# Kernel tuning notes

Hardware: AMD Instinct MI355X
Metric: run time of the kernel (lower is better)

## Reference

```python
import jax, jax.numpy as jnp
import numpy as np

N_NODES = 50000
N_EDGES = 800000
D_IN = 128
D_OUT = 128


def setup_inputs() -> dict:
    key = jax.random.key(0)
    k1, k2, k3, k4, k5 = jax.random.split(key, 5)
    H = jax.random.normal(k1, (N_NODES, D_IN), dtype=jnp.float32)
    stdv = 1.0 / np.sqrt(D_OUT)
    W = jax.random.uniform(k2, (D_IN, D_OUT), dtype=jnp.float32, minval=-stdv, maxval=stdv)
    bias = jnp.zeros((D_OUT,), dtype=jnp.float32)
    edge_vals = jax.random.uniform(k3, (N_EDGES,), dtype=jnp.float32)
    edge_rows = jax.random.randint(k4, (N_EDGES,), 0, N_NODES, dtype=jnp.int32)
    edge_cols = jax.random.randint(k5, (N_EDGES,), 0, N_NODES, dtype=jnp.int32)
    return {"H": H, "W": W, "bias": bias, "edge_vals": edge_vals,
            "edge_rows": edge_rows, "edge_cols": edge_cols}


def reference(H, W, bias, edge_vals, edge_rows, edge_cols):
    # H' = relu(A @ (H W) + b), A given as COO edge list (rows, cols, vals)
    n = H.shape[0]
    HW = H @ W  # [N, D_out]
    # SpMM: out[r] = sum_{e: row(e)=r} val(e) * HW[col(e)]
    msgs = edge_vals[:, None] * HW[edge_cols]  # [E, D_out]
    out = jax.ops.segment_sum(msgs, edge_rows, num_segments=n)
    out = out + bias
    return jax.nn.relu(out)
```

## Files before the change

kernel.cpp:

```cpp
#include <hip/hip_runtime.h>

#define D 128
#define BM 64
#define NBB 256
#define BINSH 6
#define MAXBINS 1024
#define CAPB 1536

typedef __attribute__((ext_vector_type(8))) short bf16x8;
typedef __attribute__((ext_vector_type(4))) float f32x4;

__device__ __forceinline__ unsigned short f2bf(float f) {
    unsigned u = __float_as_uint(f);
    u = (u + 0x7FFFu + ((u >> 16) & 1u)) >> 16;
    return (unsigned short)u;
}
__device__ __forceinline__ float bf2f(unsigned short h) {
    return __uint_as_float(((unsigned)h) << 16);
}

__global__ __launch_bounds__(128) void k_prepw(const float* __restrict__ W,
                                               unsigned short* __restrict__ Wt,
                                               int* __restrict__ gcnt, int nbins) {
    int nn = blockIdx.x, k = threadIdx.x;
    Wt[nn * D + k] = f2bf(W[k * D + nn]);
    int gtid = blockIdx.x * 128 + threadIdx.x;
    for (int i = gtid; i < nbins * 16; i += 128 * D) gcnt[i] = 0;
}

__global__ __launch_bounds__(256) void k_gemm_bin(const float* __restrict__ H,
                                                  const unsigned short* __restrict__ Wt,
                                                  unsigned short* __restrict__ HWb,
                                                  int n,
                                                  const int* __restrict__ rows,
                                                  const int* __restrict__ cols,
                                                  const float* __restrict__ vals,
                                                  int* __restrict__ gcnt,
                                                  int2* __restrict__ segs,
                                                  int E, int nbins, int nbb) {
    __shared__ unsigned short sA[BM * D];
    __shared__ unsigned short sB[D * D];
    const int tid = threadIdx.x;
    const int row0 = blockIdx.x * BM;

#pragma unroll
    for (int s = 0; s < 8; ++s) {
        int idx = s * 256 + tid;
        int nn = idx >> 4, cc = idx & 15;
        bf16x8 v = *reinterpret_cast<const bf16x8*>(&Wt[(size_t)idx * 8]);
        *reinterpret_cast<bf16x8*>(&sB[nn * D + ((cc ^ (nn & 7)) * 8)]) = v;
    }
#pragma unroll
    for (int s = 0; s < 4; ++s) {
        int idx = s * 256 + tid;
        int r = idx >> 4, cc = idx & 15;
        int row = row0 + r;
        float4 u0 = make_float4(0.f, 0.f, 0.f, 0.f), u1 = u0;
        if (row < n) {
            const float4* p = reinterpret_cast<const float4*>(&H[(size_t)row * D + cc * 8]);
            u0 = p[0]; u1 = p[1];
        }
        bf16x8 v;
        v[0] = (short)f2bf(u0.x); v[1] = (short)f2bf(u0.y);
        v[2] = (short)f2bf(u0.z); v[3] = (short)f2bf(u0.w);
        v[4] = (short)f2bf(u1.x); v[5] = (short)f2bf(u1.y);
        v[6] = (short)f2bf(u1.z); v[7] = (short)f2bf(u1.w);
        *reinterpret_cast<bf16x8*>(&sA[r * D + ((cc ^ (r & 7)) * 8)]) = v;
    }
    __syncthreads();

    const int w = tid >> 6, l = tid & 63;
    const int lr = l & 15, lq = l >> 4;
    f32x4 acc[8];
#pragma unroll
    for (int ct = 0; ct < 8; ++ct) acc[ct] = (f32x4){0.f, 0.f, 0.f, 0.f};

#pragma unroll
    for (int ks = 0; ks < 4; ++ks) {
        const int arow = w * 16 + lr;
        const int acc_c = (ks * 4 + lq) ^ (arow & 7);
        bf16x8 a = *reinterpret_cast<const bf16x8*>(&sA[arow * D + acc_c * 8]);
#pragma unroll
        for (int ct = 0; ct < 8; ++ct) {
            const int brow = ct * 16 + lr;
            const int bcc = (ks * 4 + lq) ^ (brow & 7);
            bf16x8 b = *reinterpret_cast<const bf16x8*>(&sB[brow * D + bcc * 8]);
            acc[ct] = __builtin_amdgcn_mfma_f32_16x16x32_bf16(a, b, acc[ct], 0, 0, 0);
        }
    }

#pragma unroll
    for (int ct = 0; ct < 8; ++ct) {
#pragma unroll
        for (int i = 0; i < 4; ++i) {
            int row = row0 + w * 16 + lq * 4 + i;
            int col = ct * 16 + lr;
            if (row < n) HWb[(size_t)row * D + col] = f2bf(acc[ct][i]);
        }
    }

    if (blockIdx.x < (unsigned)nbb) {
        __syncthreads();
        int* lcnt = reinterpret_cast<int*>(sA);
        int* loff = lcnt + MAXBINS;
        int chunk = (E + nbb - 1) / nbb;
        int s = blockIdx.x * chunk;
        int epos = s + chunk; if (epos > E) epos = E;
        for (int i = tid; i < nbins; i += 256) lcnt[i] = 0;
        __syncthreads();
        for (int e = s + tid; e < epos; e += 256)
            atomicAdd(&lcnt[rows[e] >> BINSH], 1);
        __syncthreads();
        for (int i = tid; i < nbins; i += 256) {
            int c = lcnt[i];
            int base = c ? atomicAdd(&gcnt[i * 16], c) : 0;
            loff[i] = i * CAPB + base;
            lcnt[i] = 0;
        }
        __syncthreads();
        for (int e = s + tid; e < epos; e += 256) {
            int r = rows[e];
            int c = cols[e];
            float v = vals[e];
            int bin = r >> BINSH;
            int p = atomicAdd(&lcnt[bin], 1);
            int pos = loff[bin] + p;
            if (pos < (bin + 1) * CAPB)
                segs[pos] = make_int2(((r & 63) << 16) | c, __float_as_int(v));
        }
    }
}

__global__ __launch_bounds__(512) void k_spmm(const unsigned short* __restrict__ HWb,
                                              const int* __restrict__ gcnt,
                                              const int2* __restrict__ segs,
                                              const float* __restrict__ bias,
                                              float* __restrict__ out, int n) {
    __shared__ int2 sent[CAPB];
    __shared__ int lcnt[64];
    __shared__ int loff[64];
    __shared__ int lcur[64];
    const int b = blockIdx.x;
    int cnt = gcnt[b * 16];
    if (cnt > CAPB) cnt = CAPB;
    const int2* seg = segs + (size_t)b * CAPB;

    if (threadIdx.x < 64) lcnt[threadIdx.x] = 0;
    __syncthreads();
    int2 er[3];
#pragma unroll
    for (int k = 0; k < 3; ++k) {
        int i = threadIdx.x + k * 512;
        if (i < cnt) {
            er[k] = seg[i];
            atomicAdd(&lcnt[((unsigned)er[k].x) >> 16], 1);
        }
    }
    __syncthreads();
    if (threadIdx.x < 64) {
        int v = lcnt[threadIdx.x];
        int inc = v;
#pragma unroll
        for (int o = 1; o < 64; o <<= 1) {
            int t = __shfl_up(inc, o);
            if (threadIdx.x >= o) inc += t;
        }
        loff[threadIdx.x] = inc - v;
        lcur[threadIdx.x] = inc - v;
    }
    __syncthreads();
#pragma unroll
    for (int k = 0; k < 3; ++k) {
        int i = threadIdx.x + k * 512;
        if (i < cnt) {
            int p = atomicAdd(&lcur[((unsigned)er[k].x) >> 16], 1);
            sent[p] = er[k];
        }
    }
    __syncthreads();

    const int w = threadIdx.x >> 6, lane = threadIdx.x & 63;
    const unsigned c2 = 2 * lane;
    const float2 bb = *reinterpret_cast<const float2*>(&bias[c2]);

    for (int rr = w; rr < 64; rr += 8) {
        int row = b * 64 + rr;
        if (row >= n) break;
        int s = loff[rr];
        int deg = lcnt[rr];
        float a0 = 0.f, a1 = 0.f, b0 = 0.f, b1 = 0.f;
        int t = 0;
        for (; t + 8 <= deg; t += 8) {
            int2 e0 = sent[s + t],     e1 = sent[s + t + 1];
            int2 e2 = sent[s + t + 2], e3 = sent[s + t + 3];
            int2 e4 = sent[s + t + 4], e5 = sent[s + t + 5];
            int2 e6 = sent[s + t + 6], e7 = sent[s + t + 7];
            unsigned m0 = *reinterpret_cast<const unsigned*>(&HWb[(size_t)(e0.x & 0xFFFF) * D + c2]);
            unsigned m1 = *reinterpret_cast<const unsigned*>(&HWb[(size_t)(e1.x & 0xFFFF) * D + c2]);
            unsigned m2 = *reinterpret_cast<const unsigned*>(&HWb[(size_t)(e2.x & 0xFFFF) * D + c2]);
            unsigned m3 = *reinterpret_cast<const unsigned*>(&HWb[(size_t)(e3.x & 0xFFFF) * D + c2]);
            unsigned m4 = *reinterpret_cast<const unsigned*>(&HWb[(size_t)(e4.x & 0xFFFF) * D + c2]);
            unsigned m5 = *reinterpret_cast<const unsigned*>(&HWb[(size_t)(e5.x & 0xFFFF) * D + c2]);
            unsigned m6 = *reinterpret_cast<const unsigned*>(&HWb[(size_t)(e6.x & 0xFFFF) * D + c2]);
            unsigned m7 = *reinterpret_cast<const unsigned*>(&HWb[(size_t)(e7.x & 0xFFFF) * D + c2]);
            float v0 = __int_as_float(e0.y), v1 = __int_as_float(e1.y);
            float v2 = __int_as_float(e2.y), v3 = __int_as_float(e3.y);
            float v4 = __int_as_float(e4.y), v5 = __int_as_float(e5.y);
            float v6 = __int_as_float(e6.y), v7 = __int_as_float(e7.y);
            a0 += v0 * bf2f((unsigned short)(m0 & 0xFFFF));
            a1 += v0 * bf2f((unsigned short)(m0 >> 16));
            b0 += v1 * bf2f((unsigned short)(m1 & 0xFFFF));
            b1 += v1 * bf2f((unsigned short)(m1 >> 16));
            a0 += v2 * bf2f((unsigned short)(m2 & 0xFFFF));
            a1 += v2 * bf2f((unsigned short)(m2 >> 16));
            b0 += v3 * bf2f((unsigned short)(m3 & 0xFFFF));
            b1 += v3 * bf2f((unsigned short)(m3 >> 16));
            a0 += v4 * bf2f((unsigned short)(m4 & 0xFFFF));
            a1 += v4 * bf2f((unsigned short)(m4 >> 16));
            b0 += v5 * bf2f((unsigned short)(m5 & 0xFFFF));
            b1 += v5 * bf2f((unsigned short)(m5 >> 16));
            a0 += v6 * bf2f((unsigned short)(m6 & 0xFFFF));
            a1 += v6 * bf2f((unsigned short)(m6 >> 16));
            b0 += v7 * bf2f((unsigned short)(m7 & 0xFFFF));
            b1 += v7 * bf2f((unsigned short)(m7 >> 16));
        }
        for (; t < deg; ++t) {
            int2 e = sent[s + t];
            unsigned m = *reinterpret_cast<const unsigned*>(&HWb[(size_t)(e.x & 0xFFFF) * D + c2]);
            float v = __int_as_float(e.y);
            a0 += v * bf2f((unsigned short)(m & 0xFFFF));
            a1 += v * bf2f((unsigned short)(m >> 16));
        }
        float2 o;
        o.x = fmaxf(a0 + b0 + bb.x, 0.f);
        o.y = fmaxf(a1 + b1 + bb.y, 0.f);
        *reinterpret_cast<float2*>(&out[(size_t)row * D + c2]) = o;
    }
}

__global__ void k_init_bias(const float* __restrict__ bias, float* __restrict__ out, int n) {
    int i = blockIdx.x * blockDim.x + threadIdx.x;
    if (i < n * D) out[i] = bias[i & (D - 1)];
}
__global__ void k_scatter(const unsigned short* __restrict__ HWb, const int* __restrict__ rows,
                          const int* __restrict__ cols, const float* __restrict__ vals,
                          float* __restrict__ out, int E) {
    int e = blockIdx.x * 2 + (threadIdx.x >> 7);
    int j = threadIdx.x & (D - 1);
    if (e < E) {
        int r = rows[e];
        int c = cols[e];
        float v = vals[e];
        atomicAdd(&out[(size_t)r * D + j], v * bf2f(HWb[(size_t)c * D + j]));
    }
}
__global__ void k_relu(float* __restrict__ out, int n) {
    int i = blockIdx.x * blockDim.x + threadIdx.x;
    if (i < n * D) out[i] = fmaxf(out[i], 0.f);
}

extern "C" void kernel_launch(void* const* d_in, const int* in_sizes, int n_in,
                              void* d_out, int out_size, void* d_ws, size_t ws_size,
                              hipStream_t stream) {
    const float* H         = (const float*)d_in[0];
    const float* W         = (const float*)d_in[1];
    const float* bias      = (const float*)d_in[2];
    const float* edge_vals = (const float*)d_in[3];
    const int*   edge_rows = (const int*)d_in[4];
    const int*   edge_cols = (const int*)d_in[5];
    float* out = (float*)d_out;

    const int n = in_sizes[0] / D;
    const int E = in_sizes[3];
    const int gblocks = (n + BM - 1) / BM;
    const int nbins = (n + 63) >> BINSH;
    const int nbb = (gblocks < NBB) ? gblocks : NBB;

    char* ws = (char*)d_ws;
    unsigned short* HWb = (unsigned short*)ws; ws += (size_t)n * D * sizeof(unsigned short);
    unsigned short* Wt  = (unsigned short*)ws; ws += (size_t)D * D * sizeof(unsigned short);
    int* gcnt = (int*)ws;            ws += (size_t)nbins * 16 * sizeof(int);
    int2* segs = (int2*)ws;          ws += (size_t)nbins * CAPB * sizeof(int2);
    size_t need_full = (size_t)(ws - (char*)d_ws);

    k_prepw<<<D, D, 0, stream>>>(W, Wt, gcnt, nbins);

    if (ws_size >= need_full && n < 65536 && nbins <= MAXBINS) {
        k_gemm_bin<<<gblocks, 256, 0, stream>>>(H, Wt, HWb, n,
                                                edge_rows, edge_cols, edge_vals,
                                                gcnt, segs, E, nbins, nbb);
        k_spmm<<<nbins, 512, 0, stream>>>(HWb, gcnt, segs, bias, out, n);
    } else {
        k_gemm_bin<<<gblocks, 256, 0, stream>>>(H, Wt, HWb, n,
                                                edge_rows, edge_cols, edge_vals,
                                                (int*)d_ws, (int2*)d_ws, 0, nbins, 0);
        k_init_bias<<<((size_t)n * D + 255) / 256, 256, 0, stream>>>(bias, out, n);
        k_scatter<<<(E + 1) / 2, 256, 0, stream>>>(HWb, edge_rows, edge_cols, edge_vals, out, E);
        k_relu<<<((size_t)n * D + 255) / 256, 256, 0, stream>>>(out, n);
    }
}
```

Baseline: 73.59 us.

## Split GEMM K loop into two halves to shrink LDS and vectorize output stores

The fused GEMM+binning kernel now loads H and W in two K-halves of 64, halving the shared-memory footprint (sA/sB) so more blocks can be resident per CU. It also swaps the MFMA operand order so each lane holds four consecutive output columns of one row, letting the HW output be written as 8-byte ushort4 stores instead of scalar 2-byte stores. The cost is an extra barrier and a second load phase per block. The LDS region reused by the binning step is also smaller, which may constrain the lcnt/loff arrays.

```diff
diff --git a/kernel.cpp b/kernel.cpp
--- a/kernel.cpp
+++ b/kernel.cpp
@@ -38,64 +38,72 @@
                                                   int* __restrict__ gcnt,
                                                   int2* __restrict__ segs,
                                                   int E, int nbins, int nbb) {
-    __shared__ unsigned short sA[BM * D];
-    __shared__ unsigned short sB[D * D];
+    __shared__ unsigned short sA[BM * 64];
+    __shared__ unsigned short sB[D * 64];
     const int tid = threadIdx.x;
     const int row0 = blockIdx.x * BM;
-
-#pragma unroll
-    for (int s = 0; s < 8; ++s) {
-        int idx = s * 256 + tid;
-        int nn = idx >> 4, cc = idx & 15;
-        bf16x8 v = *reinterpret_cast<const bf16x8*>(&Wt[(size_t)idx * 8]);
-        *reinterpret_cast<bf16x8*>(&sB[nn * D + ((cc ^ (nn & 7)) * 8)]) = v;
-    }
-#pragma unroll
-    for (int s = 0; s < 4; ++s) {
-        int idx = s * 256 + tid;
-        int r = idx >> 4, cc = idx & 15;
-        int row = row0 + r;
-        float4 u0 = make_float4(0.f, 0.f, 0.f, 0.f), u1 = u0;
-        if (row < n) {
-            const float4* p = reinterpret_cast<const float4*>(&H[(size_t)row * D + cc * 8]);
-            u0 = p[0]; u1 = p[1];
-        }
-        bf16x8 v;
-        v[0] = (short)f2bf(u0.x); v[1] = (short)f2bf(u0.y);
-        v[2] = (short)f2bf(u0.z); v[3] = (short)f2bf(u0.w);
-        v[4] = (short)f2bf(u1.x); v[5] = (short)f2bf(u1.y);
-        v[6] = (short)f2bf(u1.z); v[7] = (short)f2bf(u1.w);
-        *reinterpret_cast<bf16x8*>(&sA[r * D + ((cc ^ (r & 7)) * 8)]) = v;
-    }
-    __syncthreads();
-
     const int w = tid >> 6, l = tid & 63;
     const int lr = l & 15, lq = l >> 4;
+
     f32x4 acc[8];
 #pragma unroll
     for (int ct = 0; ct < 8; ++ct) acc[ct] = (f32x4){0.f, 0.f, 0.f, 0.f};
 
 #pragma unroll
-    for (int ks = 0; ks < 4; ++ks) {
-        const int arow = w * 16 + lr;
-        const int acc_c = (ks * 4 + lq) ^ (arow & 7);
-        bf16x8 a = *reinterpret_cast<const bf16x8*>(&sA[arow * D + acc_c * 8]);
-#pragma unroll
-        for (int ct = 0; ct < 8; ++ct) {
-            const int brow = ct * 16 + lr;
-            const int bcc = (ks * 4 + lq) ^ (brow & 7);
-            bf16x8 b = *reinterpret_cast<const bf16x8*>(&sB[brow * D + bcc * 8]);
-            acc[ct] = __builtin_amdgcn_mfma_f32_16x16x32_bf16(a, b, acc[ct], 0, 0, 0);
-        }
-    }
-
-#pragma unroll
-    for (int ct = 0; ct < 8; ++ct) {
-#pragma unroll
-        for (int i = 0; i < 4; ++i) {
-            int row = row0 + w * 16 + lq * 4 + i;
-            int col = ct * 16 + lr;
-            if (row < n) HWb[(size_t)row * D + col] = f2bf(acc[ct][i]);
+    for (int kt = 0; kt < 2; ++kt) {
+        if (kt) __syncthreads();
+#pragma unroll
+        for (int s = 0; s < 4; ++s) {
+            int idx = s * 256 + tid;
+            int r = idx >> 3, cc = idx & 7;
+            bf16x8 v = *reinterpret_cast<const bf16x8*>(&Wt[(size_t)r * D + kt * 64 + cc * 8]);
+            *reinterpret_cast<bf16x8*>(&sB[r * 64 + ((cc ^ (r & 7)) * 8)]) = v;
+        }
+#pragma unroll
+        for (int s = 0; s < 2; ++s) {
+            int idx = s * 256 + tid;
+            int r = idx >> 3, cc = idx & 7;
+            int row = row0 + r;
+            float4 u0 = make_float4(0.f, 0.f, 0.f, 0.f), u1 = u0;
+            if (row < n) {
+                const float4* p = reinterpret_cast<const float4*>(
+                    &H[(size_t)row * D + kt * 64 + cc * 8]);
+                u0 = p[0]; u1 = p[1];
+            }
+            bf16x8 v;
+            v[0] = (short)f2bf(u0.x); v[1] = (short)f2bf(u0.y);
+            v[2] = (short)f2bf(u0.z); v[3] = (short)f2bf(u0.w);
+            v[4] = (short)f2bf(u1.x); v[5] = (short)f2bf(u1.y);
+            v[6] = (short)f2bf(u1.z); v[7] = (short)f2bf(u1.w);
+            *reinterpret_cast<bf16x8*>(&sA[r * 64 + ((cc ^ (r & 7)) * 8)]) = v;
+        }
+        __syncthreads();
+
+#pragma unroll
+        for (int ks = 0; ks < 2; ++ks) {
+            const int arow = w * 16 + lr;
+            const int acc_c = (ks * 4 + lq) ^ (arow & 7);
+            bf16x8 a = *reinterpret_cast<const bf16x8*>(&sA[arow * 64 + acc_c * 8]);
+#pragma unroll
+            for (int ct = 0; ct < 8; ++ct) {
+                const int brow = ct * 16 + lr;
+                const int bcc = (ks * 4 + lq) ^ (brow & 7);
+                bf16x8 b = *reinterpret_cast<const bf16x8*>(&sB[brow * 64 + bcc * 8]);
+                acc[ct] = __builtin_amdgcn_mfma_f32_16x16x32_bf16(b, a, acc[ct], 0, 0, 0);
+            }
+        }
+    }
+
+    {
+        int row = row0 + w * 16 + lr;
+        if (row < n) {
+#pragma unroll
+            for (int ct = 0; ct < 8; ++ct) {
+                ushort4 o;
+                o.x = f2bf(acc[ct][0]); o.y = f2bf(acc[ct][1]);
+                o.z = f2bf(acc[ct][2]); o.w = f2bf(acc[ct][3]);
+                *reinterpret_cast<ushort4*>(&HWb[(size_t)row * D + ct * 16 + lq * 4]) = o;
+            }
         }
     }
 
```

Result: no change. 74.43 us (+1.2%).
